# Performance work log

Measured on AMD Instinct MI355X. Metric: run time of the kernel, lower is better.

Reference implementation:

```python
import jax, jax.numpy as jnp
import numpy as np

N, M, E = 20000, 5000, 320000   # nodes, hyperedges, incidence edges
HEADS, OUT, EDIM = 4, 32, 32
NEG_SLOPE = 0.2


def setup_inputs() -> dict:
    key = jax.random.key(0)
    ks = jax.random.split(key, 7)
    feat = jax.random.normal(ks[0], (N, HEADS * OUT), jnp.float32)
    edge_feat = jax.random.normal(ks[1], (E, EDIM), jnp.float32)
    H = jax.random.uniform(ks[2], (N, M), jnp.float32)
    attn_l = jax.random.normal(ks[3], (1, HEADS, OUT), jnp.float32)
    attn_m = jax.random.normal(ks[4], (1, HEADS, EDIM), jnp.float32)
    src = jax.random.randint(ks[5], (E,), 0, N, jnp.int32)
    dst = jax.random.randint(ks[6], (E,), 0, M, jnp.int32)
    return dict(feat=feat, edge_feat=edge_feat, H=H,
                attn_l=attn_l, attn_m=attn_m, src=src, dst=dst)


def _segment_softmax(e, seg, num):
    # numerically stable softmax over edges grouped by destination segment
    emax = jax.ops.segment_max(e, seg, num_segments=num)
    emax = jnp.where(jnp.isfinite(emax), emax, 0.0)  # guard empty segments
    ex = jnp.exp(e - emax[seg])
    den = jax.ops.segment_sum(ex, seg, num_segments=num)
    return ex / den[seg]


def reference(feat, edge_feat, H, attn_l, attn_m, src, dst):
    feat_src = feat.reshape(-1, HEADS, OUT)                 # [N,h,d]
    el = (feat_src * attn_l).sum(-1)                        # [N,h]
    em = (edge_feat[:, None, :] * attn_m).sum(-1)           # [E,h]
    e = el[src] + em                                        # [E,h]
    e = jnp.where(e > 0, e, NEG_SLOPE * e)                  # LeakyReLU
    a = _segment_softmax(e, dst, M)                         # edge softmax per dst
    msg = feat_src[src] * a[..., None]                      # [E,h,d]
    agg = jax.ops.segment_sum(msg, dst, num_segments=M)     # [M,h,d]
    rst = jnp.einsum('nm,mdk->ndk', H, agg)                 # [N,h,d]
    return rst.reshape(rst.shape[0], -1)
```

## Files before the change

### kernel.cpp

```cpp
#include <hip/hip_runtime.h>

#define NN 20000
#define MM 5000
#define EE 320000
#define FD 128
#define KD 5000
#define K2 5120
#define NEG 0.2f
#define BK 128
#define BUFB 65536
#define BOFF 32768
#define NKT 40
#define SPLITK 4
#define KTPS 10
#define PS4 640000

typedef __attribute__((ext_vector_type(4))) float f32x4;
typedef __attribute__((ext_vector_type(8))) short short8;

__device__ __forceinline__ unsigned int f2bf(float x){
  unsigned int u = __float_as_uint(x);
  return (u + 0x7fffu + ((u >> 16) & 1u)) >> 16;
}
__device__ __forceinline__ unsigned int cvtpk(float lo, float hi){
  unsigned int r;
  asm volatile("v_cvt_pk_bf16_f32 %0, %1, %2" : "=v"(r) : "v"(lo), "v"(hi));
  return r;
}
__device__ __forceinline__ void dma16(const void* g, void* l){
  __builtin_amdgcn_global_load_lds(
      (const __attribute__((address_space(1))) void*)g,
      (__attribute__((address_space(3))) void*)l, 16, 0, 0);
}

__global__ __launch_bounds__(256) void k_prep(const float* __restrict__ feat,
                                              const float* __restrict__ attn_l,
                                              float* __restrict__ el,
                                              unsigned int* __restrict__ fb){
  int t = threadIdx.x;
  int node = blockIdx.x*4 + (t>>6);
  int l = t & 63;
  float2 f = ((const float2*)feat)[(size_t)node*64 + l];
  fb[(size_t)node*64 + l] = cvtpk(f.x, f.y);
  float p = f.x*attn_l[2*l] + f.y*attn_l[2*l+1];
  p += __shfl_xor(p,1); p += __shfl_xor(p,2); p += __shfl_xor(p,4); p += __shfl_xor(p,8);
  if ((l&15)==0) el[node*4 + (l>>4)] = p;
}

__global__ __launch_bounds__(256) void k_count(const int* __restrict__ dst,
                                               int* __restrict__ counts){
  int e = blockIdx.x*256 + threadIdx.x;
  if (e < EE) atomicAdd(&counts[dst[e]], 1);
}

__global__ __launch_bounds__(256) void k_scan(const int* __restrict__ counts,
                                              int* __restrict__ offsets){
  __shared__ int sc[256];
  int t = threadIdx.x;
  int loc[20];
  int sum = 0;
  #pragma unroll
  for (int j=0;j<20;j++){
    int idx = t*20 + j;
    int v = (idx < MM) ? counts[idx] : 0;
    loc[j] = sum; sum += v;
  }
  sc[t] = sum; __syncthreads();
  for (int s=1; s<256; s<<=1){
    int v = 0;
    if (t >= s) v = sc[t-s];
    __syncthreads();
    if (t >= s) sc[t] += v;
    __syncthreads();
  }
  int base = sc[t] - sum;
  #pragma unroll
  for (int j=0;j<20;j++){
    int idx = t*20 + j;
    if (idx < MM) offsets[idx] = base + loc[j];
  }
  if (t == 250) offsets[MM] = base;
}

__global__ __launch_bounds__(256) void k_edge_sc(const float* __restrict__ edge_feat,
                                                 const float* __restrict__ attn_m,
                                                 const float* __restrict__ el,
                                                 const int* __restrict__ src,
                                                 const int* __restrict__ dst,
                                                 const int* __restrict__ offsets,
                                                 int* __restrict__ cursor,
                                                 float4* __restrict__ e4_s,
                                                 int* __restrict__ src_s){
  __shared__ float am[128];
  int t = threadIdx.x;
  if (t < 128) am[t] = attn_m[t];
  __syncthreads();
  int e = blockIdx.x*16 + (t>>4);
  int c = t & 15;
  float2 f = ((const float2*)edge_feat)[(size_t)e*16 + c];
  float p0 = f.x*am[0*32+2*c] + f.y*am[0*32+2*c+1];
  float p1 = f.x*am[1*32+2*c] + f.y*am[1*32+2*c+1];
  float p2 = f.x*am[2*32+2*c] + f.y*am[2*32+2*c+1];
  float p3 = f.x*am[3*32+2*c] + f.y*am[3*32+2*c+1];
  #pragma unroll
  for (int s=1; s<16; s<<=1){
    p0 += __shfl_xor(p0,s); p1 += __shfl_xor(p1,s);
    p2 += __shfl_xor(p2,s); p3 += __shfl_xor(p3,s);
  }
  if (c==0){
    float4 ev = ((const float4*)el)[src[e]];
    float4 r;
    float v;
    v = ev.x + p0; r.x = v > 0.f ? v : NEG*v;
    v = ev.y + p1; r.y = v > 0.f ? v : NEG*v;
    v = ev.z + p2; r.z = v > 0.f ? v : NEG*v;
    v = ev.w + p3; r.w = v > 0.f ? v : NEG*v;
    int d = dst[e];
    int pos = offsets[d] + atomicAdd(&cursor[d], 1);
    e4_s[pos] = r;
    src_s[pos] = src[e];
  }
}

__global__ __launch_bounds__(256) void k_agg(const float4* __restrict__ e4_s,
                                             const int* __restrict__ src_s,
                                             const unsigned int* __restrict__ fb,
                                             const int* __restrict__ offsets,
                                             unsigned short* __restrict__ aggT){
  int m = blockIdx.x;
  int t = threadIdx.x;
  if (m < (K2 - KD) && t < FD) aggT[(size_t)t*K2 + KD + m] = 0;
  int beg = offsets[m], end = offsets[m+1];
  int cnt = end - beg;
  if (cnt == 0){
    if (t < FD) aggT[(size_t)t*K2 + m] = 0;
    return;
  }
  __shared__ float accs[4][FD];
  __shared__ float dens[4][4];
  int w = t>>6, l = t&63, h = l>>4;
  float accx=0.f, accy=0.f, den=0.f;
  int i = w;
  #pragma unroll 1
  for (; i+4 < cnt; i += 8){
    float4 ev0 = e4_s[beg+i];
    float4 ev1 = e4_s[beg+i+4];
    int s0 = src_s[beg+i];
    int s1 = src_s[beg+i+4];
    unsigned int v0 = fb[(size_t)s0*64 + l];
    unsigned int v1 = fb[(size_t)s1*64 + l];
    float eh0 = (h==0)?ev0.x:((h==1)?ev0.y:((h==2)?ev0.z:ev0.w));
    float eh1 = (h==0)?ev1.x:((h==1)?ev1.y:((h==2)?ev1.z:ev1.w));
    float p0 = __expf(eh0 - 32.0f);
    float p1 = __expf(eh1 - 32.0f);
    accx += p0*__uint_as_float(v0<<16) + p1*__uint_as_float(v1<<16);
    accy += p0*__uint_as_float(v0&0xffff0000u) + p1*__uint_as_float(v1&0xffff0000u);
    den  += p0 + p1;
  }
  if (i < cnt){
    float4 ev = e4_s[beg+i];
    int s0 = src_s[beg+i];
    unsigned int v = fb[(size_t)s0*64 + l];
    float eh = (h==0)?ev.x:((h==1)?ev.y:((h==2)?ev.z:ev.w));
    float p = __expf(eh - 32.0f);
    accx += p*__uint_as_float(v<<16);
    accy += p*__uint_as_float(v&0xffff0000u);
    den  += p;
  }
  accs[w][2*l]   = accx;
  accs[w][2*l+1] = accy;
  if ((l&15)==0) dens[w][h] = den;
  __syncthreads();
  if (t < FD){
    float s = accs[0][t]+accs[1][t]+accs[2][t]+accs[3][t];
    float dn = dens[0][t>>5]+dens[1][t>>5]+dens[2][t>>5]+dens[3][t>>5];
    aggT[(size_t)t*K2 + m] = (unsigned short)f2bf(s/dn);
  }
}

__global__ __launch_bounds__(512, 2) void k_gemm(const float* __restrict__ H,
                                                 const unsigned short* __restrict__ aggT,
                                                 float* __restrict__ part){
  __shared__ char lds[2*BUFB];
  int t = threadIdx.x;
  int row0 = blockIdx.x * 64;
  int kt0 = blockIdx.y * KTPS;

  int w8 = t>>6, l = t&63;
  const size_t AMAX = (size_t)NN*KD - 4;

  int wr = (w8>>2)*32, wc = (w8&3)*32;
  int rl = l&15, kg = l>>4;
  int arowA = (wr+rl)*512;
  int arowB = (wr+16+rl)*512;
  int bcol0 = BOFF + (wc+ 0+rl)*256;
  int bcol1 = BOFF + (wc+16+rl)*256;

  f32x4 acc00={0,0,0,0}, acc01={0,0,0,0};
  f32x4 acc10={0,0,0,0}, acc11={0,0,0,0};

#define STAGE(KT, BUF)                                                        \
  { size_t kb_ = (size_t)(KT)*BK;                                             \
    _Pragma("unroll")                                                         \
    for (int j=0;j<4;j++){                \
      int r_ = row0 + w8*8 + j*2 + (l>>5);                                    \
      if (r_ > NN-1) r_ = NN-1;                                               \
      size_t s_ = (size_t)r_*KD + (size_t)((l&31) ^ (r_&15))*4 + kb_;         \
      if (s_ > AMAX) s_ = AMAX;                                               \
      dma16(H + s_, (BUF) + (w8*8 + j*2)*512);                                \
    }                                                                         \
    _Pragma("unroll")                                                         \
    for (int j=0;j<4;j++){                \
      int c_ = w8*16 + j*4 + (l>>4);                                          \
      size_t s_ = (size_t)c_*K2 + (size_t)((l&15) ^ (c_&15))*8 + kb_;         \
      dma16(aggT + s_, (BUF) + BOFF + (w8*16 + j*4)*256);                     \
    }                                                                         \
  }

#define COMP_KK(R_, KK)                                                       \
  { int gA0 = (KK)*8 + kg*2;                                                  \
    int sA0 = ((gA0  ) ^ rl) << 4;                                            \
    int sA1 = ((gA0+1) ^ rl) << 4;                                            \
    f32x4 x0_ = *(const f32x4*)(R_ + arowA + sA0);                            \
    f32x4 x1_ = *(const f32x4*)(R_ + arowA + sA1);                            \
    f32x4 y0_ = *(const f32x4*)(R_ + arowB + sA0);                            \
    f32x4 y1_ = *(const f32x4*)(R_ + arowB + sA1);                            \
    int sB_ = (((KK)*4 + kg) ^ rl) << 4;                                      \
    short8 b0_ = *(const short8*)(R_ + bcol0 + sB_);                          \
    short8 b1_ = *(const short8*)(R_ + bcol1 + sB_);                          \
    uint4 ua_, ub_;                                                           \
    ua_.x = cvtpk(x0_[0],x0_[1]); ua_.y = cvtpk(x0_[2],x0_[3]);               \
    ua_.z = cvtpk(x1_[0],x1_[1]); ua_.w = cvtpk(x1_[2],x1_[3]);               \
    ub_.x = cvtpk(y0_[0],y0_[1]); ub_.y = cvtpk(y0_[2],y0_[3]);               \
    ub_.z = cvtpk(y1_[0],y1_[1]); ub_.w = cvtpk(y1_[2],y1_[3]);               \
    short8 a0_ = *(short8*)&ua_;                                              \
    short8 a1_ = *(short8*)&ub_;                                              \
    acc00 = __builtin_amdgcn_mfma_f32_16x16x32_bf16(a0_,b0_,acc00,0,0,0);     \
    acc01 = __builtin_amdgcn_mfma_f32_16x16x32_bf16(a0_,b1_,acc01,0,0,0);     \
    acc10 = __builtin_amdgcn_mfma_f32_16x16x32_bf16(a1_,b0_,acc10,0,0,0);     \
    acc11 = __builtin_amdgcn_mfma_f32_16x16x32_bf16(a1_,b1_,acc11,0,0,0);     \
  }

  STAGE(kt0,   lds)
  STAGE(kt0+1, lds + BUFB)

  int pr = 0;
  for (int tt = 0; tt < KTPS; ++tt){
    if (tt+1 < KTPS) { asm volatile("s_waitcnt vmcnt(8)" ::: "memory"); }
    else             { asm volatile("s_waitcnt vmcnt(0)" ::: "memory"); }
    __builtin_amdgcn_s_barrier();
    { const char* R_ = lds + pr*BUFB;
      COMP_KK(R_, 0)
      COMP_KK(R_, 1)
      COMP_KK(R_, 2)
      COMP_KK(R_, 3)
    }
    __builtin_amdgcn_s_barrier();
    __builtin_amdgcn_sched_barrier(0);
    if (tt+2 < KTPS) STAGE(kt0+tt+2, lds + pr*BUFB)
    pr ^= 1;
  }
#undef STAGE
#undef COMP_KK

  float* pout = part + (size_t)blockIdx.y*NN*FD;
#define STORE(ACC, FR, FN)                                                    \
  { _Pragma("unroll")                                                         \
    for (int q=0;q<4;q++){                                                    \
      int r = row0 + wr + (FR)*16 + kg*4 + q;                                 \
      if (r < NN) pout[(size_t)r*FD + wc + (FN)*16 + rl] = ACC[q];            \
    } }
  STORE(acc00,0,0) STORE(acc01,0,1)
  STORE(acc10,1,0) STORE(acc11,1,1)
#undef STORE
}

__global__ __launch_bounds__(256) void k_reduce(const float4* __restrict__ part,
                                                float4* __restrict__ out){
  int i = blockIdx.x*256 + threadIdx.x;
  float4 a = part[i];
  float4 b = part[i + 1*PS4];
  float4 c = part[i + 2*PS4];
  float4 d = part[i + 3*PS4];
  float4 r;
  r.x = (a.x+b.x)+(c.x+d.x);
  r.y = (a.y+b.y)+(c.y+d.y);
  r.z = (a.z+b.z)+(c.z+d.z);
  r.w = (a.w+b.w)+(c.w+d.w);
  out[i] = r;
}

extern "C" void kernel_launch(void* const* d_in, const int* in_sizes, int n_in,
                              void* d_out, int out_size, void* d_ws, size_t ws_size,
                              hipStream_t stream) {
  const float* feat      = (const float*)d_in[0];
  const float* edge_feat = (const float*)d_in[1];
  const float* H         = (const float*)d_in[2];
  const float* attn_l    = (const float*)d_in[3];
  const float* attn_m    = (const float*)d_in[4];
  const int*   src       = (const int*)d_in[5];
  const int*   dst       = (const int*)d_in[6];
  float* out = (float*)d_out;

  char* w = (char*)d_ws;
  float*          el       = (float*)(w + 0);
  unsigned short* aggT     = (unsigned short*)(w + 0);
  int*            counts   = (int*)(w + 1310720);
  int*            cursor   = (int*)(w + 1331200);
  int*            offsets  = (int*)(w + 1351680);
  int*            src_s    = (int*)(w + 1372160);
  float4*         e4_s     = (float4*)(w + 2652160);
  unsigned int*   fb       = (unsigned int*)(w + 7772160);
  float*          part     = (float*)(w + 12892160);

  hipMemsetAsync(counts, 0, 2*20480, stream);

  k_prep   <<<NN/4,   256, 0, stream>>>(feat, attn_l, el, fb);
  k_count  <<<EE/256, 256, 0, stream>>>(dst, counts);
  k_scan   <<<1,      256, 0, stream>>>(counts, offsets);
  k_edge_sc<<<EE/16,  256, 0, stream>>>(edge_feat, attn_m, el, src, dst,
                                        offsets, cursor, e4_s, src_s);
  k_agg    <<<MM,     256, 0, stream>>>(e4_s, src_s, fb, offsets, aggT);
  k_gemm   <<<dim3((NN+63)/64, SPLITK), 512, 0, stream>>>(H, aggT, part);
  k_reduce <<<PS4/256, 256, 0, stream>>>((const float4*)part, (float4*)out);
}
```

Before: 216.3 us.

## Restructure GEMM: register-staged bf16 A conversion, larger row tile, 6-way split-K

The H-by-agg GEMM now loads fp32 H rows into registers, converts them to bf16 once, and writes them to LDS, replacing the DMA of raw fp32 tiles that every wave re-converted. The block tile grows to 128 rows with a 64-wide K step and a smaller LDS footprint, allowing 4 blocks per CU, and split-K goes from 4 to 6 with a matching reduce. A, B loads and compute are pipelined over two k-steps. The partial buffer is moved to overlap earlier scratch regions, which adds more partial traffic and register pressure.

```diff
diff --git a/kernel.cpp b/kernel.cpp
--- a/kernel.cpp
+++ b/kernel.cpp
@@ -7,12 +7,11 @@
 #define KD 5000
 #define K2 5120
 #define NEG 0.2f
-#define BK 128
-#define BUFB 65536
-#define BOFF 32768
-#define NKT 40
-#define SPLITK 4
-#define KTPS 10
+#define BK 64
+#define BUFB 32768
+#define BOFF 16384
+#define SPLITK 6
+#define TPS 14
 #define PS4 640000
 
 typedef __attribute__((ext_vector_type(4))) float f32x4;
@@ -178,100 +177,164 @@
   }
 }
 
-__global__ __launch_bounds__(512, 2) void k_gemm(const float* __restrict__ H,
+__global__ __launch_bounds__(512, 4) void k_gemm(const float* __restrict__ H,
                                                  const unsigned short* __restrict__ aggT,
                                                  float* __restrict__ part){
   __shared__ char lds[2*BUFB];
   int t = threadIdx.x;
-  int row0 = blockIdx.x * 64;
-  int kt0 = blockIdx.y * KTPS;
+  int row0 = blockIdx.x * 128;
+  int y = blockIdx.y;
+  int kt0 = y * TPS;
+  int NT = 80 - kt0; if (NT > TPS) NT = TPS;
+  int nsup = NT >> 1;
 
   int w8 = t>>6, l = t&63;
   const size_t AMAX = (size_t)NN*KD - 4;
 
-  int wr = (w8>>2)*32, wc = (w8&3)*32;
+  int r = t>>2, q = t&3;
+  int gr = row0 + r; if (gr > NN-1) gr = NN-1;
+  int rx7 = r & 7;
+  int gb = (q&1)*4;
+  int pq = q>>1;
+  size_t abase = (size_t)gr*KD + q*32;
+
+  int bc0 = w8*16 + 0 + (l>>3);
+  int bc1 = w8*16 + 8 + (l>>3);
+  int bgx = (l&7) ^ (l>>3);
+  size_t bs0 = (size_t)bc0*K2 + (size_t)bgx*8;
+  size_t bs1 = (size_t)bc1*K2 + (size_t)bgx*8;
+  int bd0 = BOFF + (w8*16 + 0)*128 + l*16;
+  int bd1 = BOFF + (w8*16 + 8)*128 + l*16;
+
+  int wr = (w8>>1)*32, wc = (w8&1)*64;
   int rl = l&15, kg = l>>4;
-  int arowA = (wr+rl)*512;
-  int arowB = (wr+16+rl)*512;
-  int bcol0 = BOFF + (wc+ 0+rl)*256;
-  int bcol1 = BOFF + (wc+16+rl)*256;
-
-  f32x4 acc00={0,0,0,0}, acc01={0,0,0,0};
-  f32x4 acc10={0,0,0,0}, acc11={0,0,0,0};
-
-#define STAGE(KT, BUF)                                                        \
-  { size_t kb_ = (size_t)(KT)*BK;                                             \
+  int fx7 = rl & 7;
+  int ao0 = (wr+rl)*128;
+  int ao1 = (wr+16+rl)*128;
+  int bo0 = BOFF + (wc+ 0+rl)*128;
+  int bo1 = BOFF + (wc+16+rl)*128;
+  int bo2 = BOFF + (wc+32+rl)*128;
+  int bo3 = BOFF + (wc+48+rl)*128;
+
+  f32x4 acc00={0,0,0,0}, acc01={0,0,0,0}, acc02={0,0,0,0}, acc03={0,0,0,0};
+  f32x4 acc10={0,0,0,0}, acc11={0,0,0,0}, acc12={0,0,0,0}, acc13={0,0,0,0};
+
+  float4 fA0,fA1,fA2,fA3,fA4,fA5,fA6,fA7;
+
+#define LOADA(KSUP)                                                           \
+  { size_t b_ = abase + (size_t)(KSUP);                                       \
+    size_t a_;                                                                \
+    a_=b_+ 0; if(a_>AMAX)a_=AMAX; fA0=*(const float4*)(H+a_);                 \
+    a_=b_+ 4; if(a_>AMAX)a_=AMAX; fA1=*(const float4*)(H+a_);                 \
+    a_=b_+ 8; if(a_>AMAX)a_=AMAX; fA2=*(const float4*)(H+a_);                 \
+    a_=b_+12; if(a_>AMAX)a_=AMAX; fA3=*(const float4*)(H+a_);                 \
+    a_=b_+16; if(a_>AMAX)a_=AMAX; fA4=*(const float4*)(H+a_);                 \
+    a_=b_+20; if(a_>AMAX)a_=AMAX; fA5=*(const float4*)(H+a_);                 \
+    a_=b_+24; if(a_>AMAX)a_=AMAX; fA6=*(const float4*)(H+a_);                 \
+    a_=b_+28; if(a_>AMAX)a_=AMAX; fA7=*(const float4*)(H+a_);                 \
+  }
+
+#define WRITEA(P, BUFI)                                                       \
+  if (pq == (P)){                                                             \
+    uint4 u0_,u1_,u2_,u3_;                                                    \
+    u0_.x=cvtpk(fA0.x,fA0.y); u0_.y=cvtpk(fA0.z,fA0.w);                       \
+    u0_.z=cvtpk(fA1.x,fA1.y); u0_.w=cvtpk(fA1.z,fA1.w);                       \
+    u1_.x=cvtpk(fA2.x,fA2.y); u1_.y=cvtpk(fA2.z,fA2.w);                       \
+    u1_.z=cvtpk(fA3.x,fA3.y); u1_.w=cvtpk(fA3.z,fA3.w);                       \
+    u2_.x=cvtpk(fA4.x,fA4.y); u2_.y=cvtpk(fA4.z,fA4.w);                       \
+    u2_.z=cvtpk(fA5.x,fA5.y); u2_.w=cvtpk(fA5.z,fA5.w);                       \
+    u3_.x=cvtpk(fA6.x,fA6.y); u3_.y=cvtpk(fA6.z,fA6.w);                       \
+    u3_.z=cvtpk(fA7.x,fA7.y); u3_.w=cvtpk(fA7.z,fA7.w);                       \
+    char* W_ = lds + (BUFI)*BUFB + r*128;                                     \
+    *(uint4*)(W_ + (((gb+0)^rx7)<<4)) = u0_;                                  \
+    *(uint4*)(W_ + (((gb+1)^rx7)<<4)) = u1_;                                  \
+    *(uint4*)(W_ + (((gb+2)^rx7)<<4)) = u2_;                                  \
+    *(uint4*)(W_ + (((gb+3)^rx7)<<4)) = u3_;                                  \
+  }
+
+#define DMAB(T)                                                               \
+  { size_t kb_ = (size_t)(T)*64;                                              \
+    dma16(aggT + bs0 + kb_, lds + ((T)&1)*BUFB + bd0);                        \
+    dma16(aggT + bs1 + kb_, lds + ((T)&1)*BUFB + bd1);                        \
+  }
+
+#define COMPUTE(T)                                                            \
+  { const char* R_ = lds + ((T)&1)*BUFB;                                      \
     _Pragma("unroll")                                                         \
-    for (int j=0;j<4;j++){                \
-      int r_ = row0 + w8*8 + j*2 + (l>>5);                                    \
-      if (r_ > NN-1) r_ = NN-1;                                               \
-      size_t s_ = (size_t)r_*KD + (size_t)((l&31) ^ (r_&15))*4 + kb_;         \
-      if (s_ > AMAX) s_ = AMAX;                                               \
-      dma16(H + s_, (BUF) + (w8*8 + j*2)*512);                                \
+    for (int kk=0;kk<2;kk++){                                                 \
+      int ga_ = kk*4 + kg;                                                    \
+      int sa_ = ((ga_ ^ fx7) << 4);                                           \
+      short8 a0_ = *(const short8*)(R_ + ao0 + sa_);                          \
+      short8 a1_ = *(const short8*)(R_ + ao1 + sa_);                          \
+      short8 b0_ = *(const short8*)(R_ + bo0 + sa_);                          \
+      short8 b1_ = *(const short8*)(R_ + bo1 + sa_);                          \
+      short8 b2_ = *(const short8*)(R_ + bo2 + sa_);                          \
+      short8 b3_ = *(const short8*)(R_ + bo3 + sa_);                          \
+      acc00 = __builtin_amdgcn_mfma_f32_16x16x32_bf16(a0_,b0_,acc00,0,0,0);   \
+      acc01 = __builtin_amdgcn_mfma_f32_16x16x32_bf16(a0_,b1_,acc01,0,0,0);   \
+      acc02 = __builtin_amdgcn_mfma_f32_16x16x32_bf16(a0_,b2_,acc02,0,0,0);   \
+      acc03 = __builtin_amdgcn_mfma_f32_16x16x32_bf16(a0_,b3_,acc03,0,0,0);   \
+      acc10 = __builtin_amdgcn_mfma_f32_16x16x32_bf16(a1_,b0_,acc10,0,0,0);   \
+      acc11 = __builtin_amdgcn_mfma_f32_16x16x32_bf16(a1_,b1_,acc11,0,0,0);   \
+      acc12 = __builtin_amdgcn_mfma_f32_16x16x32_bf16(a1_,b2_,acc12,0,0,0);   \
+      acc13 = __builtin_amdgcn_mfma_f32_16x16x32_bf16(a1_,b3_,acc13,0,0,0);   \
     }                                                                         \
-    _Pragma("unroll")                                                         \
-    for (int j=0;j<4;j++){                \
-      int c_ = w8*16 + j*4 + (l>>4);                                          \
-      size_t s_ = (size_t)c_*K2 + (size_t)((l&15) ^ (c_&15))*8 + kb_;         \
-      dma16(aggT + s_, (BUF) + BOFF + (w8*16 + j*4)*256);                     \
-    }                                                                         \
-  }
-
-#define COMP_KK(R_, KK)                                                       \
-  { int gA0 = (KK)*8 + kg*2;                                                  \
-    int sA0 = ((gA0  ) ^ rl) << 4;                                            \
-    int sA1 = ((gA0+1) ^ rl) << 4;                                            \
-    f32x4 x0_ = *(const f32x4*)(R_ + arowA + sA0);                            \
-    f32x4 x1_ = *(const f32x4*)(R_ + arowA + sA1);                            \
-    f32x4 y0_ = *(const f32x4*)(R_ + arowB + sA0);                            \
-    f32x4 y1_ = *(const f32x4*)(R_ + arowB + sA1);                            \
-    int sB_ = (((KK)*4 + kg) ^ rl) << 4;                                      \
-    short8 b0_ = *(const short8*)(R_ + bcol0 + sB_);                          \
-    short8 b1_ = *(const short8*)(R_ + bcol1 + sB_);                          \
-    uint4 ua_, ub_;                                                           \
-    ua_.x = cvtpk(x0_[0],x0_[1]); ua_.y = cvtpk(x0_[2],x0_[3]);               \
-    ua_.z = cvtpk(x1_[0],x1_[1]); ua_.w = cvtpk(x1_[2],x1_[3]);               \
-    ub_.x = cvtpk(y0_[0],y0_[1]); ub_.y = cvtpk(y0_[2],y0_[3]);               \
-    ub_.z = cvtpk(y1_[0],y1_[1]); ub_.w = cvtpk(y1_[2],y1_[3]);               \
-    short8 a0_ = *(short8*)&ua_;                                              \
-    short8 a1_ = *(short8*)&ub_;                                              \
-    acc00 = __builtin_amdgcn_mfma_f32_16x16x32_bf16(a0_,b0_,acc00,0,0,0);     \
-    acc01 = __builtin_amdgcn_mfma_f32_16x16x32_bf16(a0_,b1_,acc01,0,0,0);     \
-    acc10 = __builtin_amdgcn_mfma_f32_16x16x32_bf16(a1_,b0_,acc10,0,0,0);     \
-    acc11 = __builtin_amdgcn_mfma_f32_16x16x32_bf16(a1_,b1_,acc11,0,0,0);     \
-  }
-
-  STAGE(kt0,   lds)
-  STAGE(kt0+1, lds + BUFB)
-
-  int pr = 0;
-  for (int tt = 0; tt < KTPS; ++tt){
-    if (tt+1 < KTPS) { asm volatile("s_waitcnt vmcnt(8)" ::: "memory"); }
-    else             { asm volatile("s_waitcnt vmcnt(0)" ::: "memory"); }
+  }
+
+  int k0 = kt0*64;
+  LOADA(k0)
+  DMAB(kt0+0)
+  DMAB(kt0+1)
+  WRITEA(0, 0)
+  WRITEA(1, 1)
+  LOADA(k0 + 128)
+  asm volatile("s_waitcnt vmcnt(10)" ::: "memory");
+  __builtin_amdgcn_sched_barrier(0);
+  asm volatile("s_waitcnt lgkmcnt(0)" ::: "memory");
+  __builtin_amdgcn_s_barrier();
+
+  for (int s = 0; s < nsup; ++s){
+    int T0 = kt0 + 2*s;
+    COMPUTE(T0)
     __builtin_amdgcn_s_barrier();
-    { const char* R_ = lds + pr*BUFB;
-      COMP_KK(R_, 0)
-      COMP_KK(R_, 1)
-      COMP_KK(R_, 2)
-      COMP_KK(R_, 3)
+    if (s < nsup-1){
+      WRITEA(0, 0)
+      DMAB(T0+2)
+      asm volatile("s_waitcnt vmcnt(2)" ::: "memory");
+    } else {
+      asm volatile("s_waitcnt vmcnt(0)" ::: "memory");
     }
-    __builtin_amdgcn_s_barrier();
     __builtin_amdgcn_sched_barrier(0);
-    if (tt+2 < KTPS) STAGE(kt0+tt+2, lds + pr*BUFB)
-    pr ^= 1;
-  }
-#undef STAGE
-#undef COMP_KK
-
-  float* pout = part + (size_t)blockIdx.y*NN*FD;
+    COMPUTE(T0+1)
+    if (s < nsup-1){
+      __builtin_amdgcn_s_barrier();
+      WRITEA(1, 1)
+      DMAB(T0+3)
+      if (s < nsup-2){
+        LOADA(k0 + (s+2)*128)
+        asm volatile("s_waitcnt vmcnt(10)" ::: "memory");
+      } else {
+        asm volatile("s_waitcnt vmcnt(2)" ::: "memory");
+      }
+      __builtin_amdgcn_sched_barrier(0);
+      asm volatile("s_waitcnt lgkmcnt(0)" ::: "memory");
+      __builtin_amdgcn_s_barrier();
+    }
+  }
+#undef LOADA
+#undef WRITEA
+#undef DMAB
+#undef COMPUTE
+
+  float* pout = part + (size_t)y*NN*FD;
 #define STORE(ACC, FR, FN)                                                    \
   { _Pragma("unroll")                                                         \
-    for (int q=0;q<4;q++){                                                    \
-      int r = row0 + wr + (FR)*16 + kg*4 + q;                                 \
-      if (r < NN) pout[(size_t)r*FD + wc + (FN)*16 + rl] = ACC[q];            \
+    for (int p_=0;p_<4;p_++){                                                 \
+      int rr = row0 + wr + (FR)*16 + kg*4 + p_;                               \
+      if (rr < NN) pout[(size_t)rr*FD + wc + (FN)*16 + rl] = ACC[p_];         \
     } }
-  STORE(acc00,0,0) STORE(acc01,0,1)
-  STORE(acc10,1,0) STORE(acc11,1,1)
+  STORE(acc00,0,0) STORE(acc01,0,1) STORE(acc02,0,2) STORE(acc03,0,3)
+  STORE(acc10,1,0) STORE(acc11,1,1) STORE(acc12,1,2) STORE(acc13,1,3)
 #undef STORE
 }
 
@@ -282,11 +345,13 @@
   float4 b = part[i + 1*PS4];
   float4 c = part[i + 2*PS4];
   float4 d = part[i + 3*PS4];
+  float4 e = part[i + 4*PS4];
+  float4 f = part[i + 5*PS4];
   float4 r;
-  r.x = (a.x+b.x)+(c.x+d.x);
-  r.y = (a.y+b.y)+(c.y+d.y);
-  r.z = (a.z+b.z)+(c.z+d.z);
-  r.w = (a.w+b.w)+(c.w+d.w);
+  r.x = ((a.x+b.x)+(c.x+d.x))+(e.x+f.x);
+  r.y = ((a.y+b.y)+(c.y+d.y))+(e.y+f.y);
+  r.z = ((a.z+b.z)+(c.z+d.z))+(e.z+f.z);
+  r.w = ((a.w+b.w)+(c.w+d.w))+(e.w+f.w);
   out[i] = r;
 }
 
@@ -311,7 +376,7 @@
   int*            src_s    = (int*)(w + 1372160);
   float4*         e4_s     = (float4*)(w + 2652160);
   unsigned int*   fb       = (unsigned int*)(w + 7772160);
-  float*          part     = (float*)(w + 12892160);
+  float*          part     = (float*)(w + 2652160);
 
   hipMemsetAsync(counts, 0, 2*20480, stream);
 
@@ -321,6 +386,6 @@
   k_edge_sc<<<EE/16,  256, 0, stream>>>(edge_feat, attn_m, el, src, dst,
                                         offsets, cursor, e4_s, src_s);
   k_agg    <<<MM,     256, 0, stream>>>(e4_s, src_s, fb, offsets, aggT);
-  k_gemm   <<<dim3((NN+63)/64, SPLITK), 512, 0, stream>>>(H, aggT, part);
+  k_gemm   <<<dim3((NN+127)/128, SPLITK), 512, 0, stream>>>(H, aggT, part);
   k_reduce <<<PS4/256, 256, 0, stream>>>((const float4*)part, (float4*)out);
 }
```

After: 301.1 us. 39.2% more time.
